# Optimization experiments

Hardware: AMD Instinct MI355X
Metric: run time of the kernel (lower is better)

## Reference

```python
import math
import jax, jax.numpy as jnp
import numpy as np

D_MODEL = 1024
N_HEADS = 16
D_K = D_MODEL // N_HEADS
THETA = 10000.0


def setup_inputs() -> dict:
    key = jax.random.key(0)
    k1, k2, k3 = jax.random.split(key, 3)
    B, S = 2, 2048
    x = jax.random.normal(k1, (B, S, D_MODEL), dtype=jnp.float32)
    std_qkv = math.sqrt(2.0 / (D_MODEL + 3 * D_MODEL))
    std_out = math.sqrt(2.0 / (D_MODEL + D_MODEL))
    # Linear weights stored as (out_features, in_features) to match the
    # einsum '... i, o i -> ... o' contraction (trunc-normal approximated
    # by clipped normal for the reference baseline).
    w_qkv = jnp.clip(jax.random.normal(k2, (3 * D_MODEL, D_MODEL), dtype=jnp.float32) * std_qkv,
                     -3 * std_qkv, 3 * std_qkv)
    b_qkv = jnp.zeros((3 * D_MODEL,), dtype=jnp.float32)
    w_out = jnp.clip(jax.random.normal(k3, (D_MODEL, D_MODEL), dtype=jnp.float32) * std_out,
                     -3 * std_out, 3 * std_out)
    b_out = jnp.zeros((D_MODEL,), dtype=jnp.float32)
    return {"x": x, "w_qkv": w_qkv, "b_qkv": b_qkv, "w_out": w_out, "b_out": b_out}


def _rope(t, cos, sin):
    # t: (B, H, S, D_K); cos/sin: (S, D_K//2) broadcast over batch/heads.
    B, H, S, d = t.shape
    tp = t.reshape(B, H, S, d // 2, 2)
    even, odd = tp[..., 0], tp[..., 1]
    r_even = even * cos - odd * sin
    r_odd = even * sin + odd * cos
    return jnp.stack([r_even, r_odd], axis=-1).reshape(B, H, S, d)


def reference(x, w_qkv, b_qkv, w_out, b_out):
    B, S, _ = x.shape
    # QKV projection: weight is (out, in)
    qkv = jnp.einsum('bsi,oi->bso', x, w_qkv) + b_qkv  # (B, S, 3*D_MODEL)
    qkv = qkv.reshape(B, S, 3, N_HEADS, D_K).transpose(2, 0, 3, 1, 4)  # (3, B, H, S, D_K)
    q, k, v = qkv[0], qkv[1], qkv[2]

    # RoPE with default token_positions = arange(S)
    inv_freq = THETA ** (-(jnp.arange(0, D_K, 2, dtype=jnp.float32)) / D_K)  # (D_K//2,)
    ang = jnp.arange(S, dtype=jnp.float32)[:, None] * inv_freq[None, :]      # (S, D_K//2)
    cos, sin = jnp.cos(ang), jnp.sin(ang)
    q = _rope(q, cos, sin)
    k = _rope(k, cos, sin)

    # Scaled dot-product attention in fp32 with causal mask
    scale = 1.0 / math.sqrt(D_K)
    scores = jnp.einsum('bhqd,bhkd->bhqk', q.astype(jnp.float32), k.astype(jnp.float32)) * scale
    causal = jnp.tril(jnp.ones((S, S), dtype=bool))
    scores = jnp.where(causal, scores, jnp.finfo(jnp.float32).min)
    # Custom softmax: exp(x - max) / (sum + 1e-8)
    ex = jnp.exp(scores - jnp.max(scores, axis=-1, keepdims=True))
    attn = ex / (jnp.sum(ex, axis=-1, keepdims=True) + 1e-8)
    attn = attn.astype(v.dtype)

    o = jnp.einsum('bhqk,bhkd->bhqd', attn, v)           # (B, H, S, D_K)
    o = o.transpose(0, 2, 1, 3).reshape(B, S, D_MODEL)    # (B, S, D_MODEL)
    out = jnp.einsum('bsi,oi->bso', o, w_out) + b_out
    return out
```

## Files before the change

kernel.cpp:

```cpp
#include <hip/hip_runtime.h>


typedef float f32x4 __attribute__((ext_vector_type(4)));
typedef float fvec4 __attribute__((ext_vector_type(4)));
typedef __bf16 bf16x8 __attribute__((ext_vector_type(8)));
typedef unsigned int u32x4 __attribute__((ext_vector_type(4)));

#define S_SZ 2048
#define NH 16
#define DK 64

static __device__ __forceinline__ unsigned short f2bf(float f) {
  unsigned int u = __builtin_bit_cast(unsigned int, f);
  u += 0x7fffu + ((u >> 16) & 1u);
  return (unsigned short)(u >> 16);
}
static __device__ __forceinline__ float bf2f(unsigned short h) {
  unsigned int u = ((unsigned int)h) << 16;
  return __builtin_bit_cast(float, u);
}
static __device__ __forceinline__ unsigned int pk2(float a, float b) {
  return (unsigned int)f2bf(a) | ((unsigned int)f2bf(b) << 16);
}
static __device__ __forceinline__ bf16x8 ld16g(const unsigned short* p) {
  return __builtin_bit_cast(bf16x8, *(const u32x4*)p);
}
static __device__ __forceinline__ void gload_lds16(const unsigned short* g,
                                                   unsigned short* l) {
  __builtin_amdgcn_global_load_lds(
      (const __attribute__((address_space(1))) void*)g,
      (__attribute__((address_space(3))) void*)l, 16, 0, 0);
}

template <int CTRL>
static __device__ __forceinline__ float dppmov(float x) {
  return __builtin_bit_cast(
      float, __builtin_amdgcn_update_dpp(0, __builtin_bit_cast(int, x), CTRL,
                                         0xF, 0xF, true));
}
static __device__ __forceinline__ float rmax16(float x) {
  x = fmaxf(x, dppmov<0xB1>(x));
  x = fmaxf(x, dppmov<0x4E>(x));
  x = fmaxf(x, dppmov<0x141>(x));
  x = fmaxf(x, dppmov<0x140>(x));
  return x;
}
static __device__ __forceinline__ float rsum16(float x) {
  x += dppmov<0xB1>(x);
  x += dppmov<0x4E>(x);
  x += dppmov<0x141>(x);
  x += dppmov<0x140>(x);
  return x;
}

__global__ __launch_bounds__(256) void cvt_bf16(
    const float* __restrict__ x, const float* __restrict__ wq,
    const float* __restrict__ wo, unsigned short* __restrict__ xb,
    unsigned short* __restrict__ wqb, unsigned short* __restrict__ wob) {
  const int u = blockIdx.x * 256 + threadIdx.x;
  const float* src;
  unsigned short* dst;
  int idx;
  if (u < 524288) { src = x; dst = xb; idx = u; }
  else if (u < 917504) { src = wq; dst = wqb; idx = u - 524288; }
  else { src = wo; dst = wob; idx = u - 917504; }
  const fvec4* p = (const fvec4*)(src + (size_t)idx * 8);
  const fvec4 f0 = p[0], f1 = p[1];
  u32x4 o;
  o[0] = pk2(f0[0], f0[1]); o[1] = pk2(f0[2], f0[3]);
  o[2] = pk2(f1[0], f1[1]); o[3] = pk2(f1[2], f1[3]);
  *(u32x4*)(dst + (size_t)idx * 8) = o;
}

template <bool OBF16>
__global__ __launch_bounds__(256) void gemm_bf16(
    const unsigned short* __restrict__ A, const unsigned short* __restrict__ B,
    const float* __restrict__ bias, void* __restrict__ Cp, int N, int K) {
  __shared__ unsigned short As[2][4096];
  __shared__ unsigned short Bs[2][4096];
  const int t = threadIdx.x;
  const int lane = t & 63, w = t >> 6;
  const int lo = lane & 15, g = lane >> 4;
  const int wr = (w >> 1) * 64, wc = (w & 1) * 64;
  const int gx = gridDim.x;
  int o = blockIdx.y * gx + blockIdx.x;
  const int nwg = gx * gridDim.y;
  o = (o & 7) * (nwg >> 3) + (o >> 3);
  const int by = o / gx, bx = o - by * gx;
  const int bRow = by * 128, bCol = bx * 128;
  const unsigned short* ap = A + (size_t)(bRow + (t >> 2)) * K + (t & 3) * 8;
  const unsigned short* bp = B + (size_t)(bCol + (t >> 2)) * K + (t & 3) * 8;
  const size_t rK = (size_t)64 * K;
  const int wb = w * 512;
  f32x4 acc[4][4] = {};
  gload_lds16(ap, As[0] + wb);
  gload_lds16(ap + rK, As[0] + 2048 + wb);
  gload_lds16(bp, Bs[0] + wb);
  gload_lds16(bp + rK, Bs[0] + 2048 + wb);
  const int nk = K >> 5;
  for (int kt = 0; kt < nk; ++kt) {
    __syncthreads();
    if (kt + 1 < nk) {
      const int k0 = (kt + 1) << 5;
      const int nb = (kt + 1) & 1;
      gload_lds16(ap + k0, As[nb] + wb);
      gload_lds16(ap + rK + k0, As[nb] + 2048 + wb);
      gload_lds16(bp + k0, Bs[nb] + wb);
      gload_lds16(bp + rK + k0, Bs[nb] + 2048 + wb);
    }
    const unsigned short* Ac = As[kt & 1];
    const unsigned short* Bc = Bs[kt & 1];
    bf16x8 aF[4], bF[4];
#pragma unroll
    for (int m = 0; m < 4; ++m) aF[m] = ld16g(Ac + (wr + m * 16 + lo) * 32 + 8 * g);
#pragma unroll
    for (int n = 0; n < 4; ++n) bF[n] = ld16g(Bc + (wc + n * 16 + lo) * 32 + 8 * g);
    __builtin_amdgcn_s_setprio(1);
#pragma unroll
    for (int m = 0; m < 4; ++m)
#pragma unroll
      for (int n = 0; n < 4; ++n)
        acc[m][n] = __builtin_amdgcn_mfma_f32_16x16x32_bf16(aF[m], bF[n], acc[m][n], 0, 0, 0);
    __builtin_amdgcn_s_setprio(0);
  }
#pragma unroll
  for (int m = 0; m < 4; ++m) {
#pragma unroll
    for (int n = 0; n < 4; ++n) {
      const int col = bCol + wc + n * 16 + lo;
      const float bv = bias[col];
#pragma unroll
      for (int r = 0; r < 4; ++r) {
        const int row = bRow + wr + m * 16 + g * 4 + r;
        const float v = acc[m][n][r] + bv;
        if constexpr (OBF16)
          ((unsigned short*)Cp)[(size_t)row * N + col] = f2bf(v);
        else
          ((float*)Cp)[(size_t)row * N + col] = v;
      }
    }
  }
}

__global__ __launch_bounds__(256) void rope_scatter(
    const unsigned short* __restrict__ qkv, unsigned short* __restrict__ Qo,
    unsigned short* __restrict__ Ko, unsigned short* __restrict__ Vt) {
  const int t = blockIdx.x * 256 + threadIdx.x;
  const int i = t & 31;
  const int s = (t >> 5) & (S_SZ - 1);
  const int h = (t >> 16) & (NH - 1);
  const int b = t >> 20;
  const unsigned short* row = qkv + (size_t)(b * S_SZ + s) * 3072;
  const float inv = exp2f((float)i * (-13.287712379549449f / 32.0f));
  const float ang = (float)s * inv;
  float sn, cs;
  sincosf(ang, &sn, &cs);
  const unsigned int qp = *(const unsigned int*)(row + h * 64 + 2 * i);
  const unsigned int kp = *(const unsigned int*)(row + 1024 + h * 64 + 2 * i);
  const unsigned int vp = *(const unsigned int*)(row + 2048 + h * 64 + 2 * i);
  const float qe = bf2f((unsigned short)qp), qo = bf2f((unsigned short)(qp >> 16));
  const float ke = bf2f((unsigned short)kp), ko = bf2f((unsigned short)(kp >> 16));
  const size_t hb = (size_t)(b * NH + h);
  const size_t qkbase = (hb * S_SZ + s) * DK + 2 * i;
  *(unsigned int*)(Qo + qkbase) =
      pk2((qe * cs - qo * sn) * 0.125f, (qe * sn + qo * cs) * 0.125f);
  *(unsigned int*)(Ko + qkbase) = pk2(ke * cs - ko * sn, ke * sn + ko * cs);
  const size_t vb = (hb * DK + 2 * i) * S_SZ + s;
  Vt[vb] = (unsigned short)vp;
  Vt[vb + S_SZ] = (unsigned short)(vp >> 16);
}

static __device__ __forceinline__ void stage8(const unsigned short* __restrict__ gbase,
                                              int gstride, unsigned short* tile, int t) {
  const int r = t >> 3;
  const int s16 = (t & 7) ^ (r & 7);
  gload_lds16(gbase + (size_t)r * gstride + (s16 << 3), tile + (t >> 6) * 512);
}

static __device__ __forceinline__ void attn_step(
    const unsigned short* __restrict__ Kl, const unsigned short* __restrict__ Vl,
    unsigned short* __restrict__ Pw, const bf16x8 aQ0, const bf16x8 aQ1,
    const bool diag, const int wq, const int lo, const int g,
    float* __restrict__ m, float* __restrict__ lsum, f32x4* __restrict__ oacc) {
  f32x4 s[4];
  __builtin_amdgcn_s_setprio(1);
#pragma unroll
  for (int c = 0; c < 4; ++c) {
    const int kr = c * 16 + lo;
    const int sw = kr & 7;
    const bf16x8 b0 =
        __builtin_bit_cast(bf16x8, *(const u32x4*)&Kl[kr * 64 + ((g ^ sw) << 3)]);
    const bf16x8 b1 =
        __builtin_bit_cast(bf16x8, *(const u32x4*)&Kl[kr * 64 + (((4 + g) ^ sw) << 3)]);
    f32x4 z = {};
    z = __builtin_amdgcn_mfma_f32_16x16x32_bf16(aQ0, b0, z, 0, 0, 0);
    z = __builtin_amdgcn_mfma_f32_16x16x32_bf16(aQ1, b1, z, 0, 0, 0);
    s[c] = z;
  }
  __builtin_amdgcn_s_setprio(0);
  if (diag) {
#pragma unroll
    for (int c = 0; c < 4; ++c)
#pragma unroll
      for (int r = 0; r < 4; ++r)
        if ((c * 16 + lo) > (wq * 16 + g * 4 + r)) s[c][r] = -__builtin_inff();
  }
#pragma unroll
  for (int r = 0; r < 4; ++r) {
    float rm = fmaxf(fmaxf(s[0][r], s[1][r]), fmaxf(s[2][r], s[3][r]));
    rm = rmax16(rm);
    const float mn = fmaxf(m[r], rm);
    const float alpha = __expf(m[r] - mn);
    m[r] = mn;
    float rs = 0.f;
#pragma unroll
    for (int c = 0; c < 4; ++c) {
      const float p = __expf(s[c][r] - mn);
      s[c][r] = p;
      rs += p;
    }
    rs = rsum16(rs);
    lsum[r] = lsum[r] * alpha + rs;
#pragma unroll
    for (int nt = 0; nt < 4; ++nt) oacc[nt][r] *= alpha;
#pragma unroll
    for (int c = 0; c < 4; ++c) Pw[(g * 4 + r) * 72 + c * 16 + lo] = f2bf(s[c][r]);
  }
  __builtin_amdgcn_s_setprio(1);
#pragma unroll
  for (int kc = 0; kc < 2; ++kc) {
    const bf16x8 aP =
        __builtin_bit_cast(bf16x8, *(const u32x4*)&Pw[lo * 72 + kc * 32 + 8 * g]);
#pragma unroll
    for (int nt = 0; nt < 4; ++nt) {
      const int d = nt * 16 + lo;
      const bf16x8 bV = __builtin_bit_cast(
          bf16x8, *(const u32x4*)&Vl[d * 64 + (((kc * 4 + g) ^ (d & 7)) << 3)]);
      oacc[nt] = __builtin_amdgcn_mfma_f32_16x16x32_bf16(aP, bV, oacc[nt], 0, 0, 0);
    }
  }
  __builtin_amdgcn_s_setprio(0);
}

__global__ __launch_bounds__(512, 4) void flash_attn(
    const unsigned short* __restrict__ Q, const unsigned short* __restrict__ K,
    const unsigned short* __restrict__ VT, unsigned short* __restrict__ O) {
  __shared__ unsigned short Kb[2][4096];
  __shared__ unsigned short Vb[2][4096];
  __shared__ unsigned short Pl[8][1152];
  const int t = threadIdx.x;
  const int lane = t & 63, w = t >> 6;
  const int lo = lane & 15, g = lane >> 4;
  const int bh = blockIdx.y;
  const int j = blockIdx.x;
  const int qa = j, qb = 31 - j;
  const unsigned short* Qh = Q + (size_t)bh * S_SZ * DK;
  const unsigned short* Kh = K + (size_t)bh * S_SZ * DK;
  const unsigned short* Vh = VT + (size_t)bh * DK * S_SZ;

  const int wq = w & 3;
  const bool s1 = w >= 4;
  const int rowMain = (s1 ? qb : qa) * 64 + wq * 16;
  const int rowB = qb * 64 + wq * 16;
  const bf16x8 aQ0 = ld16g(Qh + (size_t)(rowMain + lo) * DK + 8 * g);
  const bf16x8 aQ1 = ld16g(Qh + (size_t)(rowMain + lo) * DK + 32 + 8 * g);
  bf16x8 aQB0 = aQ0, aQB1 = aQ1;
  if (!s1) {
    aQB0 = ld16g(Qh + (size_t)(rowB + lo) * DK + 8 * g);
    aQB1 = ld16g(Qh + (size_t)(rowB + lo) * DK + 32 + 8 * g);
  }

  float mA[4], lA[4], mB[4], lB[4];
  f32x4 oA[4] = {}, oB[4] = {};
#pragma unroll
  for (int r = 0; r < 4; ++r) {
    mA[r] = mB[r] = -__builtin_inff();
    lA[r] = lB[r] = 0.f;
  }
  unsigned short* Pw = &Pl[w][0];

  for (int i = 0; i <= 16; ++i) {
    if (i < 16) {
      stage8(Kh + (size_t)i * 64 * DK, DK, Kb[1], t);
      stage8(Vh + i * 64, S_SZ, Vb[1], t);
    }
    if (i > qa) {
      const int t0c = 15 + i - qa;
      stage8(Kh + (size_t)t0c * 64 * DK, DK, Kb[0], t);
      stage8(Vh + t0c * 64, S_SZ, Vb[0], t);
    }
    __syncthreads();
    if (s1) {
      if (i < 16) {
        attn_step(Kb[1], Vb[1], Pw, aQ0, aQ1, false, wq, lo, g, mA, lA, oA);
      } else {
        float* ml = (float*)Pw;
#pragma unroll
        for (int r = 0; r < 4; ++r) {
          ml[r * 64 + lane] = mA[r];
          ml[(4 + r) * 64 + lane] = lA[r];
        }
        float* obase = (w < 6) ? ((float*)&Kb[1][0]) + (w - 4) * 1024
                               : ((float*)&Vb[1][0]) + (w - 6) * 1024;
#pragma unroll
        for (int nt = 0; nt < 4; ++nt)
#pragma unroll
          for (int r = 0; r < 4; ++r) obase[(nt * 4 + r) * 64 + lane] = oA[nt][r];
      }
    } else {
      if (i <= qa)
        attn_step(Kb[1], Vb[1], Pw, aQ0, aQ1, i == qa, wq, lo, g, mA, lA, oA);
      else
        attn_step(Kb[0], Vb[0], Pw, aQB0, aQB1, i == 16, wq, lo, g, mB, lB, oB);
    }
    __syncthreads();
  }

  if (!s1) {
    const int b = bh >> 4, h = bh & 15;
#pragma unroll
    for (int r = 0; r < 4; ++r) {
      const float inv = 1.0f / (lA[r] + 1e-8f);
      const size_t base = ((size_t)(b * S_SZ + rowMain + g * 4 + r)) * 1024 + h * DK;
#pragma unroll
      for (int nt = 0; nt < 4; ++nt) O[base + nt * 16 + lo] = f2bf(oA[nt][r] * inv);
    }
    const float* ml = (const float*)&Pl[w + 4][0];
    const float* obase = (w < 2) ? ((const float*)&Kb[1][0]) + w * 1024
                                 : ((const float*)&Vb[1][0]) + (w - 2) * 1024;
#pragma unroll
    for (int r = 0; r < 4; ++r) {
      const float m1 = ml[r * 64 + lane], l1 = ml[(4 + r) * 64 + lane];
      const float mh = fmaxf(mB[r], m1);
      const float a0 = __expf(mB[r] - mh), a1 = __expf(m1 - mh);
      const float linv = 1.0f / (lB[r] * a0 + l1 * a1 + 1e-8f);
      const size_t base = ((size_t)(b * S_SZ + rowB + g * 4 + r)) * 1024 + h * DK;
#pragma unroll
      for (int nt = 0; nt < 4; ++nt)
        O[base + nt * 16 + lo] =
            f2bf((oB[nt][r] * a0 + obase[(nt * 4 + r) * 64 + lane] * a1) * linv);
    }
  }
}

extern "C" void kernel_launch(void* const* d_in, const int* in_sizes, int n_in,
                              void* d_out, int out_size, void* d_ws, size_t ws_size,
                              hipStream_t stream) {
  const float* x = (const float*)d_in[0];
  const float* w_qkv = (const float*)d_in[1];
  const float* b_qkv = (const float*)d_in[2];
  const float* w_out = (const float*)d_in[3];
  const float* b_out = (const float*)d_in[4];
  float* out = (float*)d_out;

  char* ws = (char*)d_ws;
  unsigned short* xb = (unsigned short*)(ws);
  unsigned short* wqb = (unsigned short*)(ws + 8388608);
  unsigned short* wob = (unsigned short*)(ws + 14680064);
  unsigned short* qkv = (unsigned short*)(ws + 16777216);
  unsigned short* kb = (unsigned short*)(ws + 41943040);
  unsigned short* vt = (unsigned short*)(ws + 50331648);
  unsigned short* qb = xb;
  unsigned short* ob = qkv;

  cvt_bf16<<<4096, 256, 0, stream>>>(x, w_qkv, w_out, xb, wqb, wob);
  {
    dim3 grid(3072 / 128, 4096 / 128);
    gemm_bf16<true><<<grid, 256, 0, stream>>>(xb, wqb, b_qkv, qkv, 3072, 1024);
  }
  rope_scatter<<<(2 * NH * S_SZ * 32) / 256, 256, 0, stream>>>(qkv, qb, kb, vt);
  {
    dim3 grid(16, 2 * NH);
    flash_attn<<<grid, 512, 0, stream>>>(qb, kb, vt, ob);
  }
  {
    dim3 grid(1024 / 128, 4096 / 128);
    gemm_bf16<false><<<grid, 256, 0, stream>>>(ob, wob, b_out, out, 1024, 1024);
  }
}
```

Baseline: 135.5 us.

## Prefetch K/V tiles one step ahead, use exp2 softmax with lazy rescaling

Double-buffers K/V tiles so the next tile loads while the current one is computed, staging the first tile before the loop and dropping one barrier per iteration. Folds log2(e) into the Q scaling so softmax uses raw v_exp_f32, and skips rescaling the running max unless it grows by more than 8. Uses hardware packed bf16 conversion and remaps blocks across heads. LDS usage doubles and the occupancy hint drops to 2 blocks per CU.

```diff
diff --git a/kernel.cpp b/kernel.cpp
--- a/kernel.cpp
+++ b/kernel.cpp
@@ -30,6 +30,16 @@
   __builtin_amdgcn_global_load_lds(
       (const __attribute__((address_space(1))) void*)g,
       (__attribute__((address_space(3))) void*)l, 16, 0, 0);
+}
+static __device__ __forceinline__ float ex2(float x) {
+  float r;
+  asm("v_exp_f32 %0, %1" : "=v"(r) : "v"(x));
+  return r;
+}
+static __device__ __forceinline__ unsigned int cvtpk(float a, float b) {
+  unsigned int r;
+  asm("v_cvt_pk_bf16_f32 %0, %1, %2" : "=v"(r) : "v"(a), "v"(b));
+  return r;
 }
 
 template <int CTRL>
@@ -162,8 +172,9 @@
   const float ke = bf2f((unsigned short)kp), ko = bf2f((unsigned short)(kp >> 16));
   const size_t hb = (size_t)(b * NH + h);
   const size_t qkbase = (hb * S_SZ + s) * DK + 2 * i;
+  const float qs = 0.18033688011112042f;
   *(unsigned int*)(Qo + qkbase) =
-      pk2((qe * cs - qo * sn) * 0.125f, (qe * sn + qo * cs) * 0.125f);
+      pk2((qe * cs - qo * sn) * qs, (qe * sn + qo * cs) * qs);
   *(unsigned int*)(Ko + qkbase) = pk2(ke * cs - ko * sn, ke * sn + ko * cs);
   const size_t vb = (hb * DK + 2 * i) * S_SZ + s;
   Vt[vb] = (unsigned short)vp;
@@ -205,26 +216,42 @@
       for (int r = 0; r < 4; ++r)
         if ((c * 16 + lo) > (wq * 16 + g * 4 + r)) s[c][r] = -__builtin_inff();
   }
+  float rm[4];
 #pragma unroll
   for (int r = 0; r < 4; ++r) {
-    float rm = fmaxf(fmaxf(s[0][r], s[1][r]), fmaxf(s[2][r], s[3][r]));
-    rm = rmax16(rm);
-    const float mn = fmaxf(m[r], rm);
-    const float alpha = __expf(m[r] - mn);
-    m[r] = mn;
+    const float v = fmaxf(fmaxf(s[0][r], s[1][r]), fmaxf(s[2][r], s[3][r]));
+    rm[r] = rmax16(v);
+  }
+  const bool grow = (rm[0] > m[0] + 8.f) | (rm[1] > m[1] + 8.f) |
+                    (rm[2] > m[2] + 8.f) | (rm[3] > m[3] + 8.f);
+  if (__any((int)grow)) {
+#pragma unroll
+    for (int r = 0; r < 4; ++r) {
+      const float mn = fmaxf(m[r], rm[r]);
+      const float alpha = ex2(m[r] - mn);
+      m[r] = mn;
+      lsum[r] *= alpha;
+#pragma unroll
+      for (int nt = 0; nt < 4; ++nt) oacc[nt][r] *= alpha;
+    }
+  }
+#pragma unroll
+  for (int r = 0; r < 4; ++r) {
     float rs = 0.f;
 #pragma unroll
     for (int c = 0; c < 4; ++c) {
-      const float p = __expf(s[c][r] - mn);
+      const float p = ex2(s[c][r] - m[r]);
       s[c][r] = p;
       rs += p;
     }
-    rs = rsum16(rs);
-    lsum[r] = lsum[r] * alpha + rs;
-#pragma unroll
-    for (int nt = 0; nt < 4; ++nt) oacc[nt][r] *= alpha;
-#pragma unroll
-    for (int c = 0; c < 4; ++c) Pw[(g * 4 + r) * 72 + c * 16 + lo] = f2bf(s[c][r]);
+    lsum[r] += rsum16(rs);
+    const unsigned int u01 = cvtpk(s[0][r], s[1][r]);
+    const unsigned int u23 = cvtpk(s[2][r], s[3][r]);
+    unsigned short* pr = Pw + (g * 4 + r) * 72 + lo;
+    pr[0] = (unsigned short)u01;
+    pr[16] = (unsigned short)(u01 >> 16);
+    pr[32] = (unsigned short)u23;
+    pr[48] = (unsigned short)(u23 >> 16);
   }
   __builtin_amdgcn_s_setprio(1);
 #pragma unroll
@@ -242,17 +269,18 @@
   __builtin_amdgcn_s_setprio(0);
 }
 
-__global__ __launch_bounds__(512, 4) void flash_attn(
+__global__ __launch_bounds__(512, 2) void flash_attn(
     const unsigned short* __restrict__ Q, const unsigned short* __restrict__ K,
     const unsigned short* __restrict__ VT, unsigned short* __restrict__ O) {
-  __shared__ unsigned short Kb[2][4096];
-  __shared__ unsigned short Vb[2][4096];
+  __shared__ unsigned short Kb[4][4096];
+  __shared__ unsigned short Vb[4][4096];
   __shared__ unsigned short Pl[8][1152];
   const int t = threadIdx.x;
   const int lane = t & 63, w = t >> 6;
   const int lo = lane & 15, g = lane >> 4;
-  const int bh = blockIdx.y;
-  const int j = blockIdx.x;
+  const int flat = blockIdx.y * 16 + blockIdx.x;
+  const int bh = ((flat & 7) << 2) | ((flat >> 3) & 3);
+  const int j = flat >> 5;
   const int qa = j, qb = 31 - j;
   const unsigned short* Qh = Q + (size_t)bh * S_SZ * DK;
   const unsigned short* Kh = K + (size_t)bh * S_SZ * DK;
@@ -279,20 +307,22 @@
   }
   unsigned short* Pw = &Pl[w][0];
 
+  stage8(Kh, DK, Kb[0], t);
+  stage8(Vh, S_SZ, Vb[0], t);
+  __syncthreads();
   for (int i = 0; i <= 16; ++i) {
-    if (i < 16) {
-      stage8(Kh + (size_t)i * 64 * DK, DK, Kb[1], t);
-      stage8(Vh + i * 64, S_SZ, Vb[1], t);
-    }
-    if (i > qa) {
-      const int t0c = 15 + i - qa;
-      stage8(Kh + (size_t)t0c * 64 * DK, DK, Kb[0], t);
-      stage8(Vh + t0c * 64, S_SZ, Vb[0], t);
-    }
-    __syncthreads();
+    if (i < 15) {
+      stage8(Kh + (size_t)(i + 1) * 64 * DK, DK, Kb[(i + 1) & 1], t);
+      stage8(Vh + (i + 1) * 64, S_SZ, Vb[(i + 1) & 1], t);
+    }
+    if (i >= qa && i <= 15) {
+      const int tile = 16 + (i - qa);
+      stage8(Kh + (size_t)tile * 64 * DK, DK, Kb[2 + ((i - qa) & 1)], t);
+      stage8(Vh + tile * 64, S_SZ, Vb[2 + ((i - qa) & 1)], t);
+    }
     if (s1) {
       if (i < 16) {
-        attn_step(Kb[1], Vb[1], Pw, aQ0, aQ1, false, wq, lo, g, mA, lA, oA);
+        attn_step(Kb[i & 1], Vb[i & 1], Pw, aQ0, aQ1, false, wq, lo, g, mA, lA, oA);
       } else {
         float* ml = (float*)Pw;
 #pragma unroll
@@ -308,10 +338,13 @@
           for (int r = 0; r < 4; ++r) obase[(nt * 4 + r) * 64 + lane] = oA[nt][r];
       }
     } else {
-      if (i <= qa)
-        attn_step(Kb[1], Vb[1], Pw, aQ0, aQ1, i == qa, wq, lo, g, mA, lA, oA);
-      else
-        attn_step(Kb[0], Vb[0], Pw, aQB0, aQB1, i == 16, wq, lo, g, mB, lB, oB);
+      if (i <= qa) {
+        attn_step(Kb[i & 1], Vb[i & 1], Pw, aQ0, aQ1, i == qa, wq, lo, g, mA, lA, oA);
+      } else {
+        const int d = i - qa - 1;
+        attn_step(Kb[2 + (d & 1)], Vb[2 + (d & 1)], Pw, aQB0, aQB1, i == 16, wq,
+                  lo, g, mB, lB, oB);
+      }
     }
     __syncthreads();
   }
@@ -332,7 +365,7 @@
     for (int r = 0; r < 4; ++r) {
       const float m1 = ml[r * 64 + lane], l1 = ml[(4 + r) * 64 + lane];
       const float mh = fmaxf(mB[r], m1);
-      const float a0 = __expf(mB[r] - mh), a1 = __expf(m1 - mh);
+      const float a0 = ex2(mB[r] - mh), a1 = ex2(m1 - mh);
       const float linv = 1.0f / (lB[r] * a0 + l1 * a1 + 1e-8f);
       const size_t base = ((size_t)(b * S_SZ + rowB + g * 4 + r)) * 1024 + h * DK;
 #pragma unroll
```

Measured after the change: 140.6 us. 3.8% more time.

## Restructure flash attention into per-wave 32-row strips reading K/V from global

Applied to the files above, without the earlier changes.

Replaces the block-cooperative LDS-staged K/V flash attention with independent per-wave strips of 32 query rows. Each wave handles two strips paired (63-p and p) to balance causal work, and loads K and V fragments directly from global memory, which removes the shared-memory staging and the block barriers. The block mapping is reordered to spread heads across CUs. The softmax uses the raw v_exp_f32 (exp2), with log2(e) folded into the Q scale. The trade-off is more global/L2 traffic, since K/V are no longer shared across waves via LDS, and no prefetch overlap.

```diff
diff --git a/kernel.cpp b/kernel.cpp
--- a/kernel.cpp
+++ b/kernel.cpp
@@ -30,6 +30,11 @@
   __builtin_amdgcn_global_load_lds(
       (const __attribute__((address_space(1))) void*)g,
       (__attribute__((address_space(3))) void*)l, 16, 0, 0);
+}
+static __device__ __forceinline__ float ex2(float x) {
+  float r;
+  asm("v_exp_f32 %0, %1" : "=v"(r) : "v"(x));
+  return r;
 }
 
 template <int CTRL>
@@ -162,185 +167,143 @@
   const float ke = bf2f((unsigned short)kp), ko = bf2f((unsigned short)(kp >> 16));
   const size_t hb = (size_t)(b * NH + h);
   const size_t qkbase = (hb * S_SZ + s) * DK + 2 * i;
+  const float qs = 0.18033688011112042f;
   *(unsigned int*)(Qo + qkbase) =
-      pk2((qe * cs - qo * sn) * 0.125f, (qe * sn + qo * cs) * 0.125f);
+      pk2((qe * cs - qo * sn) * qs, (qe * sn + qo * cs) * qs);
   *(unsigned int*)(Ko + qkbase) = pk2(ke * cs - ko * sn, ke * sn + ko * cs);
   const size_t vb = (hb * DK + 2 * i) * S_SZ + s;
   Vt[vb] = (unsigned short)vp;
   Vt[vb + S_SZ] = (unsigned short)(vp >> 16);
 }
 
-static __device__ __forceinline__ void stage8(const unsigned short* __restrict__ gbase,
-                                              int gstride, unsigned short* tile, int t) {
-  const int r = t >> 3;
-  const int s16 = (t & 7) ^ (r & 7);
-  gload_lds16(gbase + (size_t)r * gstride + (s16 << 3), tile + (t >> 6) * 512);
-}
-
-static __device__ __forceinline__ void attn_step(
-    const unsigned short* __restrict__ Kl, const unsigned short* __restrict__ Vl,
-    unsigned short* __restrict__ Pw, const bf16x8 aQ0, const bf16x8 aQ1,
-    const bool diag, const int wq, const int lo, const int g,
-    float* __restrict__ m, float* __restrict__ lsum, f32x4* __restrict__ oacc) {
-  f32x4 s[4];
-  __builtin_amdgcn_s_setprio(1);
-#pragma unroll
-  for (int c = 0; c < 4; ++c) {
-    const int kr = c * 16 + lo;
-    const int sw = kr & 7;
-    const bf16x8 b0 =
-        __builtin_bit_cast(bf16x8, *(const u32x4*)&Kl[kr * 64 + ((g ^ sw) << 3)]);
-    const bf16x8 b1 =
-        __builtin_bit_cast(bf16x8, *(const u32x4*)&Kl[kr * 64 + (((4 + g) ^ sw) << 3)]);
-    f32x4 z = {};
-    z = __builtin_amdgcn_mfma_f32_16x16x32_bf16(aQ0, b0, z, 0, 0, 0);
-    z = __builtin_amdgcn_mfma_f32_16x16x32_bf16(aQ1, b1, z, 0, 0, 0);
-    s[c] = z;
-  }
-  __builtin_amdgcn_s_setprio(0);
-  if (diag) {
-#pragma unroll
-    for (int c = 0; c < 4; ++c)
-#pragma unroll
-      for (int r = 0; r < 4; ++r)
-        if ((c * 16 + lo) > (wq * 16 + g * 4 + r)) s[c][r] = -__builtin_inff();
-  }
-#pragma unroll
-  for (int r = 0; r < 4; ++r) {
-    float rm = fmaxf(fmaxf(s[0][r], s[1][r]), fmaxf(s[2][r], s[3][r]));
-    rm = rmax16(rm);
-    const float mn = fmaxf(m[r], rm);
-    const float alpha = __expf(m[r] - mn);
-    m[r] = mn;
-    float rs = 0.f;
+static __device__ __forceinline__ void run_strip(
+    const unsigned short* __restrict__ Qh, const unsigned short* __restrict__ Kh,
+    const unsigned short* __restrict__ Vh, unsigned short* __restrict__ O,
+    unsigned short* __restrict__ Pw, const int s, const int b, const int hh,
+    const int lo, const int g) {
+  const int row0 = s * 32;
+  bf16x8 aQ[2][2];
+#pragma unroll
+  for (int mf = 0; mf < 2; ++mf)
+#pragma unroll
+    for (int kh = 0; kh < 2; ++kh)
+      aQ[mf][kh] =
+          ld16g(Qh + (size_t)(row0 + mf * 16 + lo) * DK + kh * 32 + 8 * g);
+  float m[2][4], l[2][4];
+  f32x4 o[2][4] = {};
+#pragma unroll
+  for (int mf = 0; mf < 2; ++mf)
+#pragma unroll
+    for (int r = 0; r < 4; ++r) {
+      m[mf][r] = -__builtin_inff();
+      l[mf][r] = 0.f;
+    }
+  const int ktmax = s >> 1;
+  for (int kt = 0; kt <= ktmax; ++kt) {
+    const int kbase = kt << 6;
+    f32x4 sc[2][4];
+    __builtin_amdgcn_s_setprio(1);
 #pragma unroll
     for (int c = 0; c < 4; ++c) {
-      const float p = __expf(s[c][r] - mn);
-      s[c][r] = p;
-      rs += p;
-    }
-    rs = rsum16(rs);
-    lsum[r] = lsum[r] * alpha + rs;
-#pragma unroll
-    for (int nt = 0; nt < 4; ++nt) oacc[nt][r] *= alpha;
-#pragma unroll
-    for (int c = 0; c < 4; ++c) Pw[(g * 4 + r) * 72 + c * 16 + lo] = f2bf(s[c][r]);
-  }
-  __builtin_amdgcn_s_setprio(1);
-#pragma unroll
-  for (int kc = 0; kc < 2; ++kc) {
-    const bf16x8 aP =
-        __builtin_bit_cast(bf16x8, *(const u32x4*)&Pw[lo * 72 + kc * 32 + 8 * g]);
-#pragma unroll
-    for (int nt = 0; nt < 4; ++nt) {
-      const int d = nt * 16 + lo;
-      const bf16x8 bV = __builtin_bit_cast(
-          bf16x8, *(const u32x4*)&Vl[d * 64 + (((kc * 4 + g) ^ (d & 7)) << 3)]);
-      oacc[nt] = __builtin_amdgcn_mfma_f32_16x16x32_bf16(aP, bV, oacc[nt], 0, 0, 0);
-    }
-  }
-  __builtin_amdgcn_s_setprio(0);
-}
-
-__global__ __launch_bounds__(512, 4) void flash_attn(
+      const unsigned short* kr = Kh + (size_t)(kbase + c * 16 + lo) * DK + 8 * g;
+      const bf16x8 b0 = ld16g(kr);
+      const bf16x8 b1 = ld16g(kr + 32);
+#pragma unroll
+      for (int mf = 0; mf < 2; ++mf) {
+        f32x4 z = {};
+        z = __builtin_amdgcn_mfma_f32_16x16x32_bf16(aQ[mf][0], b0, z, 0, 0, 0);
+        z = __builtin_amdgcn_mfma_f32_16x16x32_bf16(aQ[mf][1], b1, z, 0, 0, 0);
+        sc[mf][c] = z;
+      }
+    }
+    __builtin_amdgcn_s_setprio(0);
+    if (kt == ktmax) {
+#pragma unroll
+      for (int mf = 0; mf < 2; ++mf)
+#pragma unroll
+        for (int c = 0; c < 4; ++c)
+#pragma unroll
+          for (int r = 0; r < 4; ++r)
+            if ((kbase + c * 16 + lo) > (row0 + mf * 16 + g * 4 + r))
+              sc[mf][c][r] = -__builtin_inff();
+    }
+#pragma unroll
+    for (int mf = 0; mf < 2; ++mf)
+#pragma unroll
+      for (int r = 0; r < 4; ++r) {
+        float rm = fmaxf(fmaxf(sc[mf][0][r], sc[mf][1][r]),
+                         fmaxf(sc[mf][2][r], sc[mf][3][r]));
+        rm = rmax16(rm);
+        const float mn = fmaxf(m[mf][r], rm);
+        const float alpha = ex2(m[mf][r] - mn);
+        m[mf][r] = mn;
+        float rs = 0.f;
+#pragma unroll
+        for (int c = 0; c < 4; ++c) {
+          const float p = ex2(sc[mf][c][r] - mn);
+          sc[mf][c][r] = p;
+          rs += p;
+        }
+        l[mf][r] = l[mf][r] * alpha + rsum16(rs);
+#pragma unroll
+        for (int nt = 0; nt < 4; ++nt) o[mf][nt][r] *= alpha;
+        unsigned short* pr = Pw + (mf * 16 + g * 4 + r) * 72 + lo;
+        pr[0] = f2bf(sc[mf][0][r]);
+        pr[16] = f2bf(sc[mf][1][r]);
+        pr[32] = f2bf(sc[mf][2][r]);
+        pr[48] = f2bf(sc[mf][3][r]);
+      }
+    __builtin_amdgcn_s_setprio(1);
+#pragma unroll
+    for (int kc = 0; kc < 2; ++kc) {
+      bf16x8 aP[2];
+#pragma unroll
+      for (int mf = 0; mf < 2; ++mf)
+        aP[mf] = __builtin_bit_cast(
+            bf16x8, *(const u32x4*)&Pw[(mf * 16 + lo) * 72 + kc * 32 + 8 * g]);
+#pragma unroll
+      for (int nt = 0; nt < 4; ++nt) {
+        const bf16x8 bV =
+            ld16g(Vh + (size_t)(nt * 16 + lo) * S_SZ + kbase + kc * 32 + 8 * g);
+#pragma unroll
+        for (int mf = 0; mf < 2; ++mf)
+          o[mf][nt] =
+              __builtin_amdgcn_mfma_f32_16x16x32_bf16(aP[mf], bV, o[mf][nt], 0, 0, 0);
+      }
+    }
+    __builtin_amdgcn_s_setprio(0);
+  }
+#pragma unroll
+  for (int mf = 0; mf < 2; ++mf)
+#pragma unroll
+    for (int r = 0; r < 4; ++r) {
+      const float inv = 1.0f / (l[mf][r] + 1e-8f);
+      const size_t base =
+          ((size_t)(b * S_SZ + row0 + mf * 16 + g * 4 + r)) * 1024 + hh * DK;
+#pragma unroll
+      for (int nt = 0; nt < 4; ++nt)
+        O[base + nt * 16 + lo] = f2bf(o[mf][nt][r] * inv);
+    }
+}
+
+__global__ __launch_bounds__(256, 3) void flash_attn(
     const unsigned short* __restrict__ Q, const unsigned short* __restrict__ K,
     const unsigned short* __restrict__ VT, unsigned short* __restrict__ O) {
-  __shared__ unsigned short Kb[2][4096];
-  __shared__ unsigned short Vb[2][4096];
-  __shared__ unsigned short Pl[8][1152];
+  __shared__ unsigned short Pl[4][2304];
   const int t = threadIdx.x;
   const int lane = t & 63, w = t >> 6;
   const int lo = lane & 15, g = lane >> 4;
-  const int bh = blockIdx.y;
-  const int j = blockIdx.x;
-  const int qa = j, qb = 31 - j;
-  const unsigned short* Qh = Q + (size_t)bh * S_SZ * DK;
-  const unsigned short* Kh = K + (size_t)bh * S_SZ * DK;
-  const unsigned short* Vh = VT + (size_t)bh * DK * S_SZ;
-
-  const int wq = w & 3;
-  const bool s1 = w >= 4;
-  const int rowMain = (s1 ? qb : qa) * 64 + wq * 16;
-  const int rowB = qb * 64 + wq * 16;
-  const bf16x8 aQ0 = ld16g(Qh + (size_t)(rowMain + lo) * DK + 8 * g);
-  const bf16x8 aQ1 = ld16g(Qh + (size_t)(rowMain + lo) * DK + 32 + 8 * g);
-  bf16x8 aQB0 = aQ0, aQB1 = aQ1;
-  if (!s1) {
-    aQB0 = ld16g(Qh + (size_t)(rowB + lo) * DK + 8 * g);
-    aQB1 = ld16g(Qh + (size_t)(rowB + lo) * DK + 32 + 8 * g);
-  }
-
-  float mA[4], lA[4], mB[4], lB[4];
-  f32x4 oA[4] = {}, oB[4] = {};
-#pragma unroll
-  for (int r = 0; r < 4; ++r) {
-    mA[r] = mB[r] = -__builtin_inff();
-    lA[r] = lB[r] = 0.f;
-  }
+  const int fb = blockIdx.x;
+  const int h = (fb & 7) * 4 + ((fb >> 3) >> 3);
+  const int p = ((fb >> 3) & 7) * 4 + w;
+  const unsigned short* Qh = Q + (size_t)h * S_SZ * DK;
+  const unsigned short* Kh = K + (size_t)h * S_SZ * DK;
+  const unsigned short* Vh = VT + (size_t)h * DK * S_SZ;
+  const int b = h >> 4, hh = h & 15;
   unsigned short* Pw = &Pl[w][0];
 
-  for (int i = 0; i <= 16; ++i) {
-    if (i < 16) {
-      stage8(Kh + (size_t)i * 64 * DK, DK, Kb[1], t);
-      stage8(Vh + i * 64, S_SZ, Vb[1], t);
-    }
-    if (i > qa) {
-      const int t0c = 15 + i - qa;
-      stage8(Kh + (size_t)t0c * 64 * DK, DK, Kb[0], t);
-      stage8(Vh + t0c * 64, S_SZ, Vb[0], t);
-    }
-    __syncthreads();
-    if (s1) {
-      if (i < 16) {
-        attn_step(Kb[1], Vb[1], Pw, aQ0, aQ1, false, wq, lo, g, mA, lA, oA);
-      } else {
-        float* ml = (float*)Pw;
-#pragma unroll
-        for (int r = 0; r < 4; ++r) {
-          ml[r * 64 + lane] = mA[r];
-          ml[(4 + r) * 64 + lane] = lA[r];
-        }
-        float* obase = (w < 6) ? ((float*)&Kb[1][0]) + (w - 4) * 1024
-                               : ((float*)&Vb[1][0]) + (w - 6) * 1024;
-#pragma unroll
-        for (int nt = 0; nt < 4; ++nt)
-#pragma unroll
-          for (int r = 0; r < 4; ++r) obase[(nt * 4 + r) * 64 + lane] = oA[nt][r];
-      }
-    } else {
-      if (i <= qa)
-        attn_step(Kb[1], Vb[1], Pw, aQ0, aQ1, i == qa, wq, lo, g, mA, lA, oA);
-      else
-        attn_step(Kb[0], Vb[0], Pw, aQB0, aQB1, i == 16, wq, lo, g, mB, lB, oB);
-    }
-    __syncthreads();
-  }
-
-  if (!s1) {
-    const int b = bh >> 4, h = bh & 15;
-#pragma unroll
-    for (int r = 0; r < 4; ++r) {
-      const float inv = 1.0f / (lA[r] + 1e-8f);
-      const size_t base = ((size_t)(b * S_SZ + rowMain + g * 4 + r)) * 1024 + h * DK;
-#pragma unroll
-      for (int nt = 0; nt < 4; ++nt) O[base + nt * 16 + lo] = f2bf(oA[nt][r] * inv);
-    }
-    const float* ml = (const float*)&Pl[w + 4][0];
-    const float* obase = (w < 2) ? ((const float*)&Kb[1][0]) + w * 1024
-                                 : ((const float*)&Vb[1][0]) + (w - 2) * 1024;
-#pragma unroll
-    for (int r = 0; r < 4; ++r) {
-      const float m1 = ml[r * 64 + lane], l1 = ml[(4 + r) * 64 + lane];
-      const float mh = fmaxf(mB[r], m1);
-      const float a0 = __expf(mB[r] - mh), a1 = __expf(m1 - mh);
-      const float linv = 1.0f / (lB[r] * a0 + l1 * a1 + 1e-8f);
-      const size_t base = ((size_t)(b * S_SZ + rowB + g * 4 + r)) * 1024 + h * DK;
-#pragma unroll
-      for (int nt = 0; nt < 4; ++nt)
-        O[base + nt * 16 + lo] =
-            f2bf((oB[nt][r] * a0 + obase[(nt * 4 + r) * 64 + lane] * a1) * linv);
-    }
-  }
+  run_strip(Qh, Kh, Vh, O, Pw, 63 - p, b, hh, lo, g);
+  run_strip(Qh, Kh, Vh, O, Pw, p, b, hh, lo, g);
 }
 
 extern "C" void kernel_launch(void* const* d_in, const int* in_sizes, int n_in,
@@ -369,10 +332,7 @@
     gemm_bf16<true><<<grid, 256, 0, stream>>>(xb, wqb, b_qkv, qkv, 3072, 1024);
   }
   rope_scatter<<<(2 * NH * S_SZ * 32) / 256, 256, 0, stream>>>(qkv, qb, kb, vt);
-  {
-    dim3 grid(16, 2 * NH);
-    flash_attn<<<grid, 512, 0, stream>>>(qb, kb, vt, ob);
-  }
+  flash_attn<<<256, 256, 0, stream>>>(qb, kb, vt, ob);
   {
     dim3 grid(1024 / 128, 4096 / 128);
     gemm_bf16<false><<<grid, 256, 0, stream>>>(ob, wob, b_out, out, 1024, 1024);
```

New measurement: 192.0 us. +41.7%, slower.
